# Performance work log

Hardware: AMD Instinct MI355X
Metric: run time of the kernel (lower is better)

The kernel has to match this reference:

```python
import jax, jax.numpy as jnp
import numpy as np

LAM = 0.95  # config.discount_lambda


def setup_inputs() -> dict:
    key = jax.random.key(0)
    k1, k2, k3 = jax.random.split(key, 3)
    T, B = 16, 524288  # imag_horizon + 1, flattened batch*length
    reward = jax.random.normal(k1, (T, B), jnp.float32) * 0.1
    value = jax.random.normal(k2, (T, B), jnp.float32)
    # cont-head mean in [0, 1) scaled by find_discount ~ 0.997
    discount = 0.997 * jax.random.uniform(k3, (T, B), jnp.float32)
    return {"reward": reward, "value": value, "discount": discount}


def reference(reward, value, discount):
    """Faithful jax version of ImagBehavior.lambda_return.

    torch loop (i = T-2 .. 0):
        curr = acc_last * lam + value[i+1] * (1 - lam)
        curr = reward[i] + discount[i] * curr
    then flip to time order. Here expressed as a single reverse lax.scan.
    Returns target of shape [T-1, B] in time order (indices 0 .. T-2).
    """
    def step(acc, xs):
        r, d, v_next = xs
        acc = r + d * (LAM * acc + (1.0 - LAM) * v_next)
        return acc, acc

    bootstrap = value[-1]  # [B]
    xs = (reward[:-1], discount[:-1], value[1:])  # each [T-1, B]
    _, target = jax.lax.scan(step, bootstrap, xs, reverse=True)
    return target  # [T-1, B]
```

## Files before the change

### kernel.cpp

```cpp
#include <hip/hip_runtime.h>


constexpr int   T_STEPS = 16;
constexpr float LAM     = 0.95f;

__global__ __launch_bounds__(256)
void ImagBehavior_67284957659345_kernel(const float4* __restrict__ reward,
                                        const float4* __restrict__ value,
                                        const float4* __restrict__ discount,
                                        float4* __restrict__ out,
                                        int Bv ) {
    int idx = blockIdx.x * blockDim.x + threadIdx.x;
    if (idx >= Bv) return;

    float4 vnext = value[(T_STEPS - 1) * Bv + idx];
    float4 acc   = vnext;

#pragma unroll
    for (int t = T_STEPS - 2; t >= 0; --t) {
        float4 r = reward[t * Bv + idx];
        float4 d = discount[t * Bv + idx];

        acc.x = r.x + d.x * (LAM * acc.x + (1.0f - LAM) * vnext.x);
        acc.y = r.y + d.y * (LAM * acc.y + (1.0f - LAM) * vnext.y);
        acc.z = r.z + d.z * (LAM * acc.z + (1.0f - LAM) * vnext.z);
        acc.w = r.w + d.w * (LAM * acc.w + (1.0f - LAM) * vnext.w);

        out[t * Bv + idx] = acc;

        if (t > 0) {
            vnext = value[t * Bv + idx];
        }
    }
}

extern "C" void kernel_launch(void* const* d_in, const int* in_sizes, int n_in,
                              void* d_out, int out_size, void* d_ws, size_t ws_size,
                              hipStream_t stream) {
    const float4* reward   = (const float4*)d_in[0];
    const float4* value    = (const float4*)d_in[1];
    const float4* discount = (const float4*)d_in[2];
    float4*       out      = (float4*)d_out;

    const int B  = in_sizes[0] / T_STEPS;
    const int Bv = B / 4;

    const int block = 256;
    const int grid  = (Bv + block - 1) / block;

    ImagBehavior_67284957659345_kernel<<<grid, block, 0, stream>>>(
        reward, value, discount, out, Bv);
}
```

Before: 128.3 us.

## Preload all timesteps into registers and halve vector width to float2

Loads all reward, discount and value timesteps into register arrays before the recurrence, so that many memory requests are in flight at once instead of being interleaved with the dependent computation. It switches from float4 to float2 elements, doubling the thread count, and adds a minimum-blocks-per-SM hint to launch bounds. The costs are higher register pressure and narrower per-thread memory transactions.

```diff
diff --git a/kernel.cpp b/kernel.cpp
--- a/kernel.cpp
+++ b/kernel.cpp
@@ -4,46 +4,47 @@
 constexpr int   T_STEPS = 16;
 constexpr float LAM     = 0.95f;
 
-__global__ __launch_bounds__(256)
-void ImagBehavior_67284957659345_kernel(const float4* __restrict__ reward,
-                                        const float4* __restrict__ value,
-                                        const float4* __restrict__ discount,
-                                        float4* __restrict__ out,
+__global__ __launch_bounds__(256, 4)
+void ImagBehavior_67284957659345_kernel(const float2* __restrict__ reward,
+                                        const float2* __restrict__ value,
+                                        const float2* __restrict__ discount,
+                                        float2* __restrict__ out,
                                         int Bv ) {
     int idx = blockIdx.x * blockDim.x + threadIdx.x;
     if (idx >= Bv) return;
 
-    float4 vnext = value[(T_STEPS - 1) * Bv + idx];
-    float4 acc   = vnext;
+    float2 r[T_STEPS - 1];
+    float2 d[T_STEPS - 1];
+    float2 v[T_STEPS];
 
+    v[T_STEPS - 1] = value[(T_STEPS - 1) * Bv + idx];
 #pragma unroll
     for (int t = T_STEPS - 2; t >= 0; --t) {
-        float4 r = reward[t * Bv + idx];
-        float4 d = discount[t * Bv + idx];
+        r[t] = reward[t * Bv + idx];
+        d[t] = discount[t * Bv + idx];
+        if (t >= 1) v[t] = value[t * Bv + idx];
+    }
 
-        acc.x = r.x + d.x * (LAM * acc.x + (1.0f - LAM) * vnext.x);
-        acc.y = r.y + d.y * (LAM * acc.y + (1.0f - LAM) * vnext.y);
-        acc.z = r.z + d.z * (LAM * acc.z + (1.0f - LAM) * vnext.z);
-        acc.w = r.w + d.w * (LAM * acc.w + (1.0f - LAM) * vnext.w);
-
+    float2 acc = v[T_STEPS - 1];
+#pragma unroll
+    for (int t = T_STEPS - 2; t >= 0; --t) {
+        const float2 vn = v[t + 1];
+        acc.x = r[t].x + d[t].x * (LAM * acc.x + (1.0f - LAM) * vn.x);
+        acc.y = r[t].y + d[t].y * (LAM * acc.y + (1.0f - LAM) * vn.y);
         out[t * Bv + idx] = acc;
-
-        if (t > 0) {
-            vnext = value[t * Bv + idx];
-        }
     }
 }
 
 extern "C" void kernel_launch(void* const* d_in, const int* in_sizes, int n_in,
                               void* d_out, int out_size, void* d_ws, size_t ws_size,
                               hipStream_t stream) {
-    const float4* reward   = (const float4*)d_in[0];
-    const float4* value    = (const float4*)d_in[1];
-    const float4* discount = (const float4*)d_in[2];
-    float4*       out      = (float4*)d_out;
+    const float2* reward   = (const float2*)d_in[0];
+    const float2* value    = (const float2*)d_in[1];
+    const float2* discount = (const float2*)d_in[2];
+    float2*       out      = (float2*)d_out;
 
     const int B  = in_sizes[0] / T_STEPS;
-    const int Bv = B / 4;
+    const int Bv = B / 2;
 
     const int block = 256;
     const int grid  = (Bv + block - 1) / block;
```

After: 128.0 us. About the same (-0.2%).

## Use scalar per-element threads with software-prefetched loads instead of float4

Applied to the files above, without the earlier changes.

Switches from one float4 column group per thread to one scalar column per thread, quadrupling the thread count. It also adds explicit one-step-ahead register prefetching of reward, discount and value. The aim is more memory-level parallelism and occupancy to hide load latency. In exchange each thread issues narrower loads and stores, adding instruction count.

```diff
diff --git a/kernel.cpp b/kernel.cpp
--- a/kernel.cpp
+++ b/kernel.cpp
@@ -5,49 +5,52 @@
 constexpr float LAM     = 0.95f;
 
 __global__ __launch_bounds__(256)
-void ImagBehavior_67284957659345_kernel(const float4* __restrict__ reward,
-                                        const float4* __restrict__ value,
-                                        const float4* __restrict__ discount,
-                                        float4* __restrict__ out,
-                                        int Bv ) {
-    int idx = blockIdx.x * blockDim.x + threadIdx.x;
-    if (idx >= Bv) return;
+void ImagBehavior_67284957659345_kernel(const float* __restrict__ reward,
+                                        const float* __restrict__ value,
+                                        const float* __restrict__ discount,
+                                        float* __restrict__ out,
+                                        int B) {
+    int i = blockIdx.x * blockDim.x + threadIdx.x;
+    if (i >= B) return;
 
-    float4 vnext = value[(T_STEPS - 1) * Bv + idx];
-    float4 acc   = vnext;
+    float vnext = value[(T_STEPS - 1) * B + i];
+    float acc   = vnext;
+    float rr = reward  [(T_STEPS - 2) * B + i];
+    float dd = discount[(T_STEPS - 2) * B + i];
+    float vv = value   [(T_STEPS - 2) * B + i];
 
 #pragma unroll
     for (int t = T_STEPS - 2; t >= 0; --t) {
-        float4 r = reward[t * Bv + idx];
-        float4 d = discount[t * Bv + idx];
+        float r_n = 0.f, d_n = 0.f, v_n = 0.f;
+        if (t > 0) {
+            r_n = reward  [(t - 1) * B + i];
+            d_n = discount[(t - 1) * B + i];
+            v_n = value   [(t - 1) * B + i];
+        }
 
-        acc.x = r.x + d.x * (LAM * acc.x + (1.0f - LAM) * vnext.x);
-        acc.y = r.y + d.y * (LAM * acc.y + (1.0f - LAM) * vnext.y);
-        acc.z = r.z + d.z * (LAM * acc.z + (1.0f - LAM) * vnext.z);
-        acc.w = r.w + d.w * (LAM * acc.w + (1.0f - LAM) * vnext.w);
+        acc = rr + dd * (LAM * acc + (1.0f - LAM) * vnext);
+        out[t * B + i] = acc;
 
-        out[t * Bv + idx] = acc;
-
-        if (t > 0) {
-            vnext = value[t * Bv + idx];
-        }
+        vnext = vv;
+        rr = r_n;
+        dd = d_n;
+        vv = v_n;
     }
 }
 
 extern "C" void kernel_launch(void* const* d_in, const int* in_sizes, int n_in,
                               void* d_out, int out_size, void* d_ws, size_t ws_size,
                               hipStream_t stream) {
-    const float4* reward   = (const float4*)d_in[0];
-    const float4* value    = (const float4*)d_in[1];
-    const float4* discount = (const float4*)d_in[2];
-    float4*       out      = (float4*)d_out;
+    const float* reward   = (const float*)d_in[0];
+    const float* value    = (const float*)d_in[1];
+    const float* discount = (const float*)d_in[2];
+    float*       out      = (float*)d_out;
 
-    const int B  = in_sizes[0] / T_STEPS;
-    const int Bv = B / 4;
+    const int B = in_sizes[0] / T_STEPS;
 
     const int block = 256;
-    const int grid  = (Bv + block - 1) / block;
+    const int grid  = (B + block - 1) / block;
 
     ImagBehavior_67284957659345_kernel<<<grid, block, 0, stream>>>(
-        reward, value, discount, out, Bv);
+        reward, value, discount, out, B);
 }
```

After: 129.8 us. Within noise of the previous version (+1.2%).
